# Performance work log

Measured on AMD Instinct MI355X. Metric: run time of the kernel, lower is better.

Reference implementation:

```python
import jax, jax.numpy as jnp
import numpy as np

N_NODES = 50000
N_EDGES = 800000
DIM = 128
BN_EPS = 1e-5  # torch.nn.BatchNorm1d default


def _lin_init(k, fan_in, fan_out):
    kw, kb = jax.random.split(k)
    s = 1.0 / np.sqrt(fan_in)
    W = jax.random.uniform(kw, (fan_in, fan_out), jnp.float32, -s, s)
    b = jax.random.uniform(kb, (fan_out,), jnp.float32, -s, s)
    return W, b


def setup_inputs() -> dict:
    key = jax.random.key(0)
    ks = jax.random.split(key, 8)
    d = {}
    d['h'] = jax.random.normal(ks[0], (N_NODES, DIM), jnp.float32)
    d['e'] = jax.random.normal(ks[1], (N_EDGES, DIM), jnp.float32)
    d['src'] = jax.random.randint(ks[2], (N_EDGES,), 0, N_NODES)
    d['dst'] = jax.random.randint(ks[3], (N_EDGES,), 0, N_NODES)
    # mlp_atom: Linear(128,128) -> ReLU -> Linear(128,128)
    d['Wa1'], d['ba1'] = _lin_init(ks[4], DIM, DIM)
    d['Wa2'], d['ba2'] = _lin_init(ks[5], DIM, DIM)
    # mlp_bond
    d['Wb1'], d['bb1'] = _lin_init(ks[6], DIM, DIM)
    d['Wb2'], d['bb2'] = _lin_init(ks[7], DIM, DIM)
    # BatchNorm1d affine params
    d['gamma_a'] = jnp.ones((DIM,), jnp.float32)
    d['beta_a'] = jnp.zeros((DIM,), jnp.float32)
    d['gamma_b'] = jnp.ones((DIM,), jnp.float32)
    d['beta_b'] = jnp.zeros((DIM,), jnp.float32)
    return d


def _mlp(x, W1, b1, W2, b2):
    return jax.nn.relu(x @ W1 + b1) @ W2 + b2


def _bn(x, gamma, beta):
    # training-mode batch norm over the node/edge axis
    mu = jnp.mean(x, axis=0)
    var = jnp.var(x, axis=0)
    return (x - mu) * jax.lax.rsqrt(var + BN_EPS) * gamma + beta


def reference(h, e, src, dst, Wa1, ba1, Wa2, ba2, Wb1, bb1, Wb2, bb2,
              gamma_a, beta_a, gamma_b, beta_b):
    # --- bond (edge) update: GIN-style sum of endpoint atom feats + bond feat
    me = h[src] + h[dst] + e                      # [E, D] irregular gather
    e_new = _bn(_mlp(me, Wb1, bb1, Wb2, bb2), gamma_b, beta_b)
    e_new = e_new + e                             # residual (dropout=Identity)
    # --- atom (node) update: sum-aggregate incident bond feats
    agg = jax.ops.segment_sum(e_new, dst, num_segments=N_NODES)  # [N, D] scatter
    h_new = _bn(_mlp(h + agg, Wa1, ba1, Wa2, ba2), gamma_a, beta_a)
    h_new = h_new + h                             # residual
    return h_new, e_new
```

## Files before the change

### kernel.cpp

```cpp
#include <hip/hip_runtime.h>
#include <cstddef>

#define NN 50000
#define NE 800000
#define D 128
#define BN_EPS 1e-5f

typedef __attribute__((ext_vector_type(8))) short bf16x8;
typedef __attribute__((ext_vector_type(4))) float f32x4;

union FragU { int4 i; bf16x8 v; };

__device__ __forceinline__ unsigned short f2bf(float x) {
    unsigned u = __float_as_uint(x);
    return (unsigned short)((u + 0x7fffu + ((u >> 16) & 1u)) >> 16);
}
__device__ __forceinline__ float bf2f(unsigned short b) {
    return __uint_as_float(((unsigned)b) << 16);
}
__device__ __forceinline__ unsigned pk2(float a, float b) {
    return (unsigned)f2bf(a) | ((unsigned)f2bf(b) << 16);
}

__global__ __launch_bounds__(256) void wprep_kernel(
    const float* __restrict__ W, unsigned short* __restrict__ Wt)
{
    const int idx = blockIdx.x * 256 + threadIdx.x;
    const int j  = idx & 7;
    const int l  = (idx >> 3) & 63;
    const int ks = (idx >> 9) & 3;
    const int ct = (idx >> 11) & 7;
    const int n  = 16 * ct + (l & 15);
    const int k  = 32 * ks + ((l >> 4) << 3) + j;
    Wt[idx] = f2bf(W[k * 128 + n]);
}

template<int MODE>
__global__ __launch_bounds__(256, 4) void mlp_mfma_kernel(
    const float* __restrict__ h, const float* __restrict__ e_or_agg,
    const int* __restrict__ src, const int* __restrict__ dst,
    const unsigned short* __restrict__ Wt1, const float* __restrict__ b1,
    const unsigned short* __restrict__ Wt2, const float* __restrict__ b2,
    float* __restrict__ x2out, float* __restrict__ stats)
{
    __shared__ __align__(16) unsigned short W1L[16384];
    __shared__ float red[1024];

    const int tid  = threadIdx.x;
    const int lane = tid & 63;
    const int w    = tid >> 6;
    const int g    = lane >> 4;
    const int m    = lane & 15;
    const long r0  = (long)blockIdx.x * 64;

    {
        int4* dp = (int4*)W1L;
        const int4* sp = (const int4*)Wt1;
#pragma unroll
        for (int i = 0; i < 8; ++i) dp[tid + 256 * i] = sp[tid + 256 * i];
    }
    __syncthreads();

    const long rowg = r0 + 16 * w + m;
    long rowl = rowg;
    if (MODE == 1) rowl = (rowl < NN) ? rowl : (NN - 1);

    const float *pa, *pb, *pc;
    if (MODE == 0) {
        pa = e_or_agg + (size_t)rowg * D;
        pb = h + (size_t)src[rowg] * D;
        pc = h + (size_t)dst[rowg] * D;
    } else {
        pa = h + (size_t)rowl * D;
        pb = e_or_agg + (size_t)rowl * D;
        pc = nullptr;
    }

    FragU xh[4], xl[4];
#pragma unroll
    for (int ks = 0; ks < 4; ++ks) {
        const int c = 32 * ks + 8 * g;
        const float4 aa = *(const float4*)(pa + c);
        const float4 ab = *(const float4*)(pa + c + 4);
        const float4 ba = *(const float4*)(pb + c);
        const float4 bb = *(const float4*)(pb + c + 4);
        float xs[8];
        xs[0] = aa.x + ba.x; xs[1] = aa.y + ba.y; xs[2] = aa.z + ba.z; xs[3] = aa.w + ba.w;
        xs[4] = ab.x + bb.x; xs[5] = ab.y + bb.y; xs[6] = ab.z + bb.z; xs[7] = ab.w + bb.w;
        if (MODE == 0) {
            const float4 ca = *(const float4*)(pc + c);
            const float4 cb = *(const float4*)(pc + c + 4);
            xs[0] += ca.x; xs[1] += ca.y; xs[2] += ca.z; xs[3] += ca.w;
            xs[4] += cb.x; xs[5] += cb.y; xs[6] += cb.z; xs[7] += cb.w;
        }
        const unsigned h0 = pk2(xs[0], xs[1]), h1 = pk2(xs[2], xs[3]);
        const unsigned h2 = pk2(xs[4], xs[5]), h3 = pk2(xs[6], xs[7]);
        xh[ks].i = make_int4(h0, h1, h2, h3);
        float lo[8];
        lo[0] = xs[0] - bf2f((unsigned short)h0);  lo[1] = xs[1] - bf2f((unsigned short)(h0 >> 16));
        lo[2] = xs[2] - bf2f((unsigned short)h1);  lo[3] = xs[3] - bf2f((unsigned short)(h1 >> 16));
        lo[4] = xs[4] - bf2f((unsigned short)h2);  lo[5] = xs[5] - bf2f((unsigned short)(h2 >> 16));
        lo[6] = xs[6] - bf2f((unsigned short)h3);  lo[7] = xs[7] - bf2f((unsigned short)(h3 >> 16));
        xl[ks].i = make_int4(pk2(lo[0], lo[1]), pk2(lo[2], lo[3]),
                             pk2(lo[4], lo[5]), pk2(lo[6], lo[7]));
    }

    const bf16x8* W1f = (const bf16x8*)W1L;
    f32x4 acc[8];
#pragma unroll
    for (int ct = 0; ct < 8; ++ct) acc[ct] = (f32x4){0.f, 0.f, 0.f, 0.f};
#pragma unroll
    for (int ct = 0; ct < 8; ++ct)
#pragma unroll
        for (int ks = 0; ks < 4; ++ks) {
            const bf16x8 wf = W1f[(ct * 4 + ks) * 64 + lane];
            acc[ct] = __builtin_amdgcn_mfma_f32_16x16x32_bf16(wf, xh[ks].v, acc[ct], 0, 0, 0);
            acc[ct] = __builtin_amdgcn_mfma_f32_16x16x32_bf16(wf, xl[ks].v, acc[ct], 0, 0, 0);
        }

    unsigned yh[8][2], yl[8][2];
#pragma unroll
    for (int ct = 0; ct < 8; ++ct) {
        const float4 bv = *(const float4*)(b1 + 16 * ct + 4 * g);
        const float y0 = fmaxf(acc[ct][0] + bv.x, 0.f);
        const float y1 = fmaxf(acc[ct][1] + bv.y, 0.f);
        const float y2 = fmaxf(acc[ct][2] + bv.z, 0.f);
        const float y3 = fmaxf(acc[ct][3] + bv.w, 0.f);
        yh[ct][0] = pk2(y0, y1);  yh[ct][1] = pk2(y2, y3);
        const float l0 = y0 - bf2f((unsigned short)yh[ct][0]);
        const float l1 = y1 - bf2f((unsigned short)(yh[ct][0] >> 16));
        const float l2 = y2 - bf2f((unsigned short)yh[ct][1]);
        const float l3 = y3 - bf2f((unsigned short)(yh[ct][1] >> 16));
        yl[ct][0] = pk2(l0, l1);  yl[ct][1] = pk2(l2, l3);
    }

    FragU ah[4], al[4];
    const int sA = ((g & 1) << 5) | m;
    const int sB = sA + 16;
    const bool gh = (g >> 1) != 0;
#pragma unroll
    for (int ks = 0; ks < 4; ++ks) {
        int p, q, w0, w1, w2, w3;
        p = __shfl((int)yh[2*ks][0], sA); q = __shfl((int)yh[2*ks+1][0], sA); w0 = gh ? q : p;
        p = __shfl((int)yh[2*ks][1], sA); q = __shfl((int)yh[2*ks+1][1], sA); w1 = gh ? q : p;
        p = __shfl((int)yh[2*ks][0], sB); q = __shfl((int)yh[2*ks+1][0], sB); w2 = gh ? q : p;
        p = __shfl((int)yh[2*ks][1], sB); q = __shfl((int)yh[2*ks+1][1], sB); w3 = gh ? q : p;
        ah[ks].i = make_int4(w0, w1, w2, w3);
        p = __shfl((int)yl[2*ks][0], sA); q = __shfl((int)yl[2*ks+1][0], sA); w0 = gh ? q : p;
        p = __shfl((int)yl[2*ks][1], sA); q = __shfl((int)yl[2*ks+1][1], sA); w1 = gh ? q : p;
        p = __shfl((int)yl[2*ks][0], sB); q = __shfl((int)yl[2*ks+1][0], sB); w2 = gh ? q : p;
        p = __shfl((int)yl[2*ks][1], sB); q = __shfl((int)yl[2*ks+1][1], sB); w3 = gh ? q : p;
        al[ks].i = make_int4(w0, w1, w2, w3);
    }

    const bf16x8* W2f = (const bf16x8*)Wt2;
    f32x4 acc2[8];
#pragma unroll
    for (int ct = 0; ct < 8; ++ct) acc2[ct] = (f32x4){0.f, 0.f, 0.f, 0.f};
#pragma unroll
    for (int ct = 0; ct < 8; ++ct)
#pragma unroll
        for (int ks = 0; ks < 4; ++ks) {
            const bf16x8 wf = W2f[(ct * 4 + ks) * 64 + lane];
            acc2[ct] = __builtin_amdgcn_mfma_f32_16x16x32_bf16(ah[ks].v, wf, acc2[ct], 0, 0, 0);
            acc2[ct] = __builtin_amdgcn_mfma_f32_16x16x32_bf16(al[ks].v, wf, acc2[ct], 0, 0, 0);
        }

#pragma unroll
    for (int ct = 0; ct < 8; ++ct) {
        const float b2c = b2[16 * ct + m];
        float s = 0.f, q = 0.f;
#pragma unroll
        for (int r = 0; r < 4; ++r) {
            const long grow = r0 + 16 * w + 4 * g + r;
            if (MODE == 0 || grow < NN) {
                const float z = acc2[ct][r] + b2c;
                x2out[(size_t)grow * D + 16 * ct + m] = z;
                s += z; q += z * z;
            }
        }
        s += __shfl_xor(s, 16); s += __shfl_xor(s, 32);
        q += __shfl_xor(q, 16); q += __shfl_xor(q, 32);
        if (g == 0) {
            red[w * 128 + 16 * ct + m]       = s;
            red[512 + w * 128 + 16 * ct + m] = q;
        }
    }
    __syncthreads();
    if (tid < 128) {
        const float s = red[tid] + red[128 + tid] + red[256 + tid] + red[384 + tid];
        const float q = red[512 + tid] + red[640 + tid] + red[768 + tid] + red[896 + tid];
        unsafeAtomicAdd(&stats[tid], s);
        unsafeAtomicAdd(&stats[128 + tid], q);
    }
}

__global__ void bn_finalize_kernel(float* __restrict__ stats,
                                   const float* __restrict__ gamma,
                                   const float* __restrict__ beta,
                                   float inv_count)
{
    const int c = threadIdx.x;
    if (c < D) {
        const float mu  = stats[c] * inv_count;
        const float var = stats[128 + c] * inv_count - mu * mu;
        const float sc  = rsqrtf(var + BN_EPS) * gamma[c];
        stats[256 + c] = sc;
        stats[384 + c] = beta[c] - mu * sc;
    }
}

__global__ __launch_bounds__(256) void hist_kernel(
    const int* __restrict__ dst, int* __restrict__ cnt)
{
    const int i = blockIdx.x * 256 + threadIdx.x;
    if (i < NE) atomicAdd(&cnt[dst[i]], 1);
}

__global__ __launch_bounds__(1024) void scan_kernel(
    const int* __restrict__ cnt, int* __restrict__ off)
{
    __shared__ int part[1024];
    const int t = threadIdx.x;
    const int SEG = (NN + 1023) / 1024;
    const int base = t * SEG;

    int s = 0;
    for (int i = 0; i < SEG; ++i) {
        const int idx = base + i;
        if (idx < NN) s += cnt[idx];
    }
    part[t] = s;
    __syncthreads();
    for (int d = 1; d < 1024; d <<= 1) {
        int v = (t >= d) ? part[t - d] : 0;
        __syncthreads();
        part[t] += v;
        __syncthreads();
    }
    int run = (t > 0) ? part[t - 1] : 0;
    for (int i = 0; i < SEG; ++i) {
        const int idx = base + i;
        if (idx < NN) { off[idx] = run; run += cnt[idx]; }
    }
    if (t == 1023) off[NN] = part[1023];
}

__global__ __launch_bounds__(256) void csr_scatter_kernel(
    const int* __restrict__ dst, const int* __restrict__ off,
    int* __restrict__ cnt, int* __restrict__ csr)
{
    const int i = blockIdx.x * 256 + threadIdx.x;
    if (i < NE) {
        const int d = dst[i];
        const int p = atomicSub(&cnt[d], 1) - 1;
        csr[off[d] + p] = i;
    }
}

__global__ __launch_bounds__(256) void apply_gather_kernel(
    const float* __restrict__ e, const float* __restrict__ stats,
    const int* __restrict__ off, const int* __restrict__ csr,
    float* __restrict__ eout, float* __restrict__ agg)
{
    const int node = blockIdx.x * 4 + (threadIdx.x >> 6);
    const int lane = threadIdx.x & 63;
    const int c0   = lane * 2;
    if (node >= NN) return;

    const float2 sc = *(const float2*)(stats + 256 + c0);
    const float2 sh = *(const float2*)(stats + 384 + c0);
    float2 acc = make_float2(0.f, 0.f);
    const int jb = off[node], je = off[node + 1];
    for (int j = jb; j < je; ++j) {
        const int eidx = csr[j];
        const size_t base = (size_t)eidx * D + c0;
        const float2 x  = *(const float2*)(eout + base);
        const float2 ev = *(const float2*)(e + base);
        float2 v;
        v.x = fmaf(x.x, sc.x, sh.x) + ev.x;
        v.y = fmaf(x.y, sc.y, sh.y) + ev.y;
        *(float2*)(eout + base) = v;
        acc.x += v.x;
        acc.y += v.y;
    }
    *(float2*)(agg + (size_t)node * D + c0) = acc;
}

__global__ __launch_bounds__(256) void node_apply_kernel(
    const float* __restrict__ h, const float* __restrict__ stats,
    float* __restrict__ hout)
{
    const int gid = blockIdx.x * 256 + threadIdx.x;
    const int c0  = (gid & 31) * 4;
    const size_t base = (size_t)(gid >> 5) * D + c0;

    const float4 sc = *(const float4*)(stats + 256 + c0);
    const float4 sh = *(const float4*)(stats + 384 + c0);
    const float4 x  = *(const float4*)(hout + base);
    const float4 hv = *(const float4*)(h + base);
    float4 v;
    v.x = fmaf(x.x, sc.x, sh.x) + hv.x;
    v.y = fmaf(x.y, sc.y, sh.y) + hv.y;
    v.z = fmaf(x.z, sc.z, sh.z) + hv.z;
    v.w = fmaf(x.w, sc.w, sh.w) + hv.w;
    *(float4*)(hout + base) = v;
}

extern "C" void kernel_launch(void* const* d_in, const int* in_sizes, int n_in,
                              void* d_out, int out_size, void* d_ws, size_t ws_size,
                              hipStream_t stream)
{
    const float* h   = (const float*)d_in[0];
    const float* e   = (const float*)d_in[1];
    const int*   src = (const int*)d_in[2];
    const int*   dst = (const int*)d_in[3];
    const float* Wa1 = (const float*)d_in[4];
    const float* ba1 = (const float*)d_in[5];
    const float* Wa2 = (const float*)d_in[6];
    const float* ba2 = (const float*)d_in[7];
    const float* Wb1 = (const float*)d_in[8];
    const float* bb1 = (const float*)d_in[9];
    const float* Wb2 = (const float*)d_in[10];
    const float* bb2 = (const float*)d_in[11];
    const float* ga  = (const float*)d_in[12];
    const float* bea = (const float*)d_in[13];
    const float* gb  = (const float*)d_in[14];
    const float* beb = (const float*)d_in[15];

    float* out  = (float*)d_out;
    float* hnew = out;
    float* enew = out + (size_t)NN * D;

    float* ws     = (float*)d_ws;
    float* estats = ws;
    float* nstats = ws + 512;
    int*   icnt   = (int*)(ws + 1024);
    int*   ioff   = icnt + NN;
    unsigned short* wtb1 = (unsigned short*)(ioff + NN + 1 + 3);
    unsigned short* wtb2 = wtb1 + 16384;
    unsigned short* wta1 = wtb2 + 16384;
    unsigned short* wta2 = wta1 + 16384;
    int*   icsr  = (int*)(wta2 + 16384);
    float* agg   = (float*)(icsr + NE);

    hipMemsetAsync(d_ws, 0, (size_t)(1024 + NN) * sizeof(float), stream);

    wprep_kernel<<<64, 256, 0, stream>>>(Wb1, wtb1);
    wprep_kernel<<<64, 256, 0, stream>>>(Wb2, wtb2);
    wprep_kernel<<<64, 256, 0, stream>>>(Wa1, wta1);
    wprep_kernel<<<64, 256, 0, stream>>>(Wa2, wta2);

    hist_kernel<<<(NE + 255) / 256, 256, 0, stream>>>(dst, icnt);
    scan_kernel<<<1, 1024, 0, stream>>>(icnt, ioff);
    csr_scatter_kernel<<<(NE + 255) / 256, 256, 0, stream>>>(dst, ioff, icnt, icsr);

    mlp_mfma_kernel<0><<<NE / 64, 256, 0, stream>>>(h, e, src, dst,
                                                    wtb1, bb1, wtb2, bb2,
                                                    enew , estats);
    bn_finalize_kernel<<<1, 128, 0, stream>>>(estats, gb, beb, 1.0f / NE);
    apply_gather_kernel<<<(NN + 3) / 4, 256, 0, stream>>>(e, estats, ioff, icsr,
                                                          enew, agg);

    mlp_mfma_kernel<1><<<(NN + 63) / 64, 256, 0, stream>>>(h, agg, nullptr, nullptr,
                                                           wta1, ba1, wta2, ba2,
                                                           hnew , nstats);
    bn_finalize_kernel<<<1, 128, 0, stream>>>(nstats, ga, bea, 1.0f / NN);
    node_apply_kernel<<<(NN * 32) / 256, 256, 0, stream>>>(h, nstats, hnew);
}
```

Measured before the change: 868.4 us.

## Process four row tiles per wave with double-buffered gather loads and LDS-resident W2

Each block now handles 256 rows: every wave runs four 16-row tiles. The raw gather loads for the next tile are issued before computing the current one (two register buffers), which hides the latency of the irregular loads. W2 is also staged in LDS alongside W1, and the BN partial sums are accumulated across tiles, so there are fewer blocks, fewer atomics and less repeated weight staging. The cost is heavy register use: launch bounds drop to 2 blocks per CU and 48 float4 raw buffers are held, so occupancy falls and spilling is possible. The node kernel also gets coarser work with a tail of clamped rows.

```diff
diff --git a/kernel.cpp b/kernel.cpp
--- a/kernel.cpp
+++ b/kernel.cpp
@@ -35,8 +35,135 @@
     Wt[idx] = f2bf(W[k * 128 + n]);
 }
 
+#define LOAD_TILE(TT, RAW)                                                     \
+    {                                                                          \
+        long rowg = r0w + (TT) * 16 + m;                                       \
+        if (MODE == 1 && rowg >= NN) rowg = NN - 1;                            \
+        const float *pa, *pb, *pc = nullptr;                                   \
+        if (MODE == 0) {                                                       \
+            pa = e_or_agg + (size_t)rowg * D;                                  \
+            pb = h + (size_t)src[rowg] * D;                                    \
+            pc = h + (size_t)dst[rowg] * D;                                    \
+        } else {                                                               \
+            pa = h + (size_t)rowg * D;                                         \
+            pb = e_or_agg + (size_t)rowg * D;                                  \
+        }                                                                      \
+        _Pragma("unroll")                                                      \
+        for (int ks = 0; ks < 4; ++ks) {                                       \
+            const int c = 32 * ks + 8 * g;                                     \
+            RAW[ks * 6 + 0] = *(const float4*)(pa + c);                        \
+            RAW[ks * 6 + 1] = *(const float4*)(pa + c + 4);                    \
+            RAW[ks * 6 + 2] = *(const float4*)(pb + c);                        \
+            RAW[ks * 6 + 3] = *(const float4*)(pb + c + 4);                    \
+            if (MODE == 0) {                                                   \
+                RAW[ks * 6 + 4] = *(const float4*)(pc + c);                    \
+                RAW[ks * 6 + 5] = *(const float4*)(pc + c + 4);                \
+            }                                                                  \
+        }                                                                      \
+    }
+
+#define COMPUTE_TILE(TT, RAW)                                                  \
+    {                                                                          \
+        FragU xh[4], xl[4];                                                    \
+        _Pragma("unroll")                                                      \
+        for (int ks = 0; ks < 4; ++ks) {                                       \
+            const float4 aa = RAW[ks * 6 + 0], ab = RAW[ks * 6 + 1];           \
+            const float4 ba = RAW[ks * 6 + 2], bb = RAW[ks * 6 + 3];           \
+            float xs[8];                                                       \
+            xs[0] = aa.x + ba.x; xs[1] = aa.y + ba.y;                          \
+            xs[2] = aa.z + ba.z; xs[3] = aa.w + ba.w;                          \
+            xs[4] = ab.x + bb.x; xs[5] = ab.y + bb.y;                          \
+            xs[6] = ab.z + bb.z; xs[7] = ab.w + bb.w;                          \
+            if (MODE == 0) {                                                   \
+                const float4 ca = RAW[ks * 6 + 4], cb = RAW[ks * 6 + 5];       \
+                xs[0] += ca.x; xs[1] += ca.y; xs[2] += ca.z; xs[3] += ca.w;    \
+                xs[4] += cb.x; xs[5] += cb.y; xs[6] += cb.z; xs[7] += cb.w;    \
+            }                                                                  \
+            const unsigned h0 = pk2(xs[0], xs[1]), h1 = pk2(xs[2], xs[3]);     \
+            const unsigned h2 = pk2(xs[4], xs[5]), h3 = pk2(xs[6], xs[7]);     \
+            xh[ks].i = make_int4(h0, h1, h2, h3);                              \
+            xl[ks].i = make_int4(                                              \
+                pk2(xs[0] - bf2f((unsigned short)h0),                          \
+                    xs[1] - bf2f((unsigned short)(h0 >> 16))),                 \
+                pk2(xs[2] - bf2f((unsigned short)h1),                          \
+                    xs[3] - bf2f((unsigned short)(h1 >> 16))),                 \
+                pk2(xs[4] - bf2f((unsigned short)h2),                          \
+                    xs[5] - bf2f((unsigned short)(h2 >> 16))),                 \
+                pk2(xs[6] - bf2f((unsigned short)h3),                          \
+                    xs[7] - bf2f((unsigned short)(h3 >> 16))));                \
+        }                                                                      \
+        f32x4 acc[8];                                                          \
+        _Pragma("unroll")                                                      \
+        for (int ct = 0; ct < 8; ++ct) acc[ct] = (f32x4){0.f, 0.f, 0.f, 0.f}; \
+        _Pragma("unroll")                                                      \
+        for (int ct = 0; ct < 8; ++ct)                                         \
+            _Pragma("unroll")                                                  \
+            for (int ks = 0; ks < 4; ++ks) {                                   \
+                const bf16x8 wf = W1f[(ct * 4 + ks) * 64 + lane];              \
+                acc[ct] = __builtin_amdgcn_mfma_f32_16x16x32_bf16(             \
+                    wf, xh[ks].v, acc[ct], 0, 0, 0);                           \
+                acc[ct] = __builtin_amdgcn_mfma_f32_16x16x32_bf16(             \
+                    wf, xl[ks].v, acc[ct], 0, 0, 0);                           \
+            }                                                                  \
+        unsigned yh[8][2], yl[8][2];                                           \
+        _Pragma("unroll")                                                      \
+        for (int ct = 0; ct < 8; ++ct) {                                       \
+            const float4 bv = *(const float4*)(b1 + 16 * ct + 4 * g);          \
+            const float y0 = fmaxf(acc[ct][0] + bv.x, 0.f);                    \
+            const float y1 = fmaxf(acc[ct][1] + bv.y, 0.f);                    \
+            const float y2 = fmaxf(acc[ct][2] + bv.z, 0.f);                    \
+            const float y3 = fmaxf(acc[ct][3] + bv.w, 0.f);                    \
+            yh[ct][0] = pk2(y0, y1);  yh[ct][1] = pk2(y2, y3);                 \
+            yl[ct][0] = pk2(y0 - bf2f((unsigned short)yh[ct][0]),              \
+                            y1 - bf2f((unsigned short)(yh[ct][0] >> 16)));     \
+            yl[ct][1] = pk2(y2 - bf2f((unsigned short)yh[ct][1]),              \
+                            y3 - bf2f((unsigned short)(yh[ct][1] >> 16)));     \
+        }                                                                      \
+        FragU ah[4], al[4];                                                    \
+        _Pragma("unroll")                                                      \
+        for (int ks = 0; ks < 4; ++ks) {                                       \
+            int p, q, w0, w1, w2, w3;                                          \
+            p = __shfl((int)yh[2*ks][0], sA); q = __shfl((int)yh[2*ks+1][0], sA); w0 = gh ? q : p; \
+            p = __shfl((int)yh[2*ks][1], sA); q = __shfl((int)yh[2*ks+1][1], sA); w1 = gh ? q : p; \
+            p = __shfl((int)yh[2*ks][0], sB); q = __shfl((int)yh[2*ks+1][0], sB); w2 = gh ? q : p; \
+            p = __shfl((int)yh[2*ks][1], sB); q = __shfl((int)yh[2*ks+1][1], sB); w3 = gh ? q : p; \
+            ah[ks].i = make_int4(w0, w1, w2, w3);                              \
+            p = __shfl((int)yl[2*ks][0], sA); q = __shfl((int)yl[2*ks+1][0], sA); w0 = gh ? q : p; \
+            p = __shfl((int)yl[2*ks][1], sA); q = __shfl((int)yl[2*ks+1][1], sA); w1 = gh ? q : p; \
+            p = __shfl((int)yl[2*ks][0], sB); q = __shfl((int)yl[2*ks+1][0], sB); w2 = gh ? q : p; \
+            p = __shfl((int)yl[2*ks][1], sB); q = __shfl((int)yl[2*ks+1][1], sB); w3 = gh ? q : p; \
+            al[ks].i = make_int4(w0, w1, w2, w3);                              \
+        }                                                                      \
+        f32x4 acc2[8];                                                         \
+        _Pragma("unroll")                                                      \
+        for (int ct = 0; ct < 8; ++ct) acc2[ct] = (f32x4){0.f, 0.f, 0.f, 0.f};\
+        _Pragma("unroll")                                                      \
+        for (int ct = 0; ct < 8; ++ct)                                         \
+            _Pragma("unroll")                                                  \
+            for (int ks = 0; ks < 4; ++ks) {                                   \
+                const bf16x8 wf = W2f[(ct * 4 + ks) * 64 + lane];              \
+                acc2[ct] = __builtin_amdgcn_mfma_f32_16x16x32_bf16(            \
+                    ah[ks].v, wf, acc2[ct], 0, 0, 0);                          \
+                acc2[ct] = __builtin_amdgcn_mfma_f32_16x16x32_bf16(            \
+                    al[ks].v, wf, acc2[ct], 0, 0, 0);                          \
+            }                                                                  \
+        _Pragma("unroll")                                                      \
+        for (int ct = 0; ct < 8; ++ct) {                                       \
+            const float b2c = b2[16 * ct + m];                                 \
+            _Pragma("unroll")                                                  \
+            for (int r = 0; r < 4; ++r) {                                      \
+                const long grow = r0w + (TT) * 16 + 4 * g + r;                 \
+                if (MODE == 0 || grow < NN) {                                  \
+                    const float z = acc2[ct][r] + b2c;                         \
+                    x2out[(size_t)grow * D + 16 * ct + m] = z;                 \
+                    sAcc[ct] += z; qAcc[ct] += z * z;                          \
+                }                                                              \
+            }                                                                  \
+        }                                                                      \
+    }
+
 template<int MODE>
-__global__ __launch_bounds__(256, 4) void mlp_mfma_kernel(
+__global__ __launch_bounds__(256, 2) void mlp_mfma_kernel(
     const float* __restrict__ h, const float* __restrict__ e_or_agg,
     const int* __restrict__ src, const int* __restrict__ dst,
     const unsigned short* __restrict__ Wt1, const float* __restrict__ b1,
@@ -44,6 +171,7 @@
     float* __restrict__ x2out, float* __restrict__ stats)
 {
     __shared__ __align__(16) unsigned short W1L[16384];
+    __shared__ __align__(16) unsigned short W2L[16384];
     __shared__ float red[1024];
 
     const int tid  = threadIdx.x;
@@ -51,134 +179,42 @@
     const int w    = tid >> 6;
     const int g    = lane >> 4;
     const int m    = lane & 15;
-    const long r0  = (long)blockIdx.x * 64;
+    const long r0w = (long)blockIdx.x * 256 + 64 * w;
 
     {
-        int4* dp = (int4*)W1L;
-        const int4* sp = (const int4*)Wt1;
+        int4* d1 = (int4*)W1L;  const int4* s1 = (const int4*)Wt1;
+        int4* d2 = (int4*)W2L;  const int4* s2 = (const int4*)Wt2;
 #pragma unroll
-        for (int i = 0; i < 8; ++i) dp[tid + 256 * i] = sp[tid + 256 * i];
+        for (int i = 0; i < 8; ++i) {
+            d1[tid + 256 * i] = s1[tid + 256 * i];
+            d2[tid + 256 * i] = s2[tid + 256 * i];
+        }
     }
     __syncthreads();
 
-    const long rowg = r0 + 16 * w + m;
-    long rowl = rowg;
-    if (MODE == 1) rowl = (rowl < NN) ? rowl : (NN - 1);
-
-    const float *pa, *pb, *pc;
-    if (MODE == 0) {
-        pa = e_or_agg + (size_t)rowg * D;
-        pb = h + (size_t)src[rowg] * D;
-        pc = h + (size_t)dst[rowg] * D;
-    } else {
-        pa = h + (size_t)rowl * D;
-        pb = e_or_agg + (size_t)rowl * D;
-        pc = nullptr;
-    }
-
-    FragU xh[4], xl[4];
-#pragma unroll
-    for (int ks = 0; ks < 4; ++ks) {
-        const int c = 32 * ks + 8 * g;
-        const float4 aa = *(const float4*)(pa + c);
-        const float4 ab = *(const float4*)(pa + c + 4);
-        const float4 ba = *(const float4*)(pb + c);
-        const float4 bb = *(const float4*)(pb + c + 4);
-        float xs[8];
-        xs[0] = aa.x + ba.x; xs[1] = aa.y + ba.y; xs[2] = aa.z + ba.z; xs[3] = aa.w + ba.w;
-        xs[4] = ab.x + bb.x; xs[5] = ab.y + bb.y; xs[6] = ab.z + bb.z; xs[7] = ab.w + bb.w;
-        if (MODE == 0) {
-            const float4 ca = *(const float4*)(pc + c);
-            const float4 cb = *(const float4*)(pc + c + 4);
-            xs[0] += ca.x; xs[1] += ca.y; xs[2] += ca.z; xs[3] += ca.w;
-            xs[4] += cb.x; xs[5] += cb.y; xs[6] += cb.z; xs[7] += cb.w;
-        }
-        const unsigned h0 = pk2(xs[0], xs[1]), h1 = pk2(xs[2], xs[3]);
-        const unsigned h2 = pk2(xs[4], xs[5]), h3 = pk2(xs[6], xs[7]);
-        xh[ks].i = make_int4(h0, h1, h2, h3);
-        float lo[8];
-        lo[0] = xs[0] - bf2f((unsigned short)h0);  lo[1] = xs[1] - bf2f((unsigned short)(h0 >> 16));
-        lo[2] = xs[2] - bf2f((unsigned short)h1);  lo[3] = xs[3] - bf2f((unsigned short)(h1 >> 16));
-        lo[4] = xs[4] - bf2f((unsigned short)h2);  lo[5] = xs[5] - bf2f((unsigned short)(h2 >> 16));
-        lo[6] = xs[6] - bf2f((unsigned short)h3);  lo[7] = xs[7] - bf2f((unsigned short)(h3 >> 16));
-        xl[ks].i = make_int4(pk2(lo[0], lo[1]), pk2(lo[2], lo[3]),
-                             pk2(lo[4], lo[5]), pk2(lo[6], lo[7]));
-    }
-
     const bf16x8* W1f = (const bf16x8*)W1L;
-    f32x4 acc[8];
-#pragma unroll
-    for (int ct = 0; ct < 8; ++ct) acc[ct] = (f32x4){0.f, 0.f, 0.f, 0.f};
-#pragma unroll
-    for (int ct = 0; ct < 8; ++ct)
-#pragma unroll
-        for (int ks = 0; ks < 4; ++ks) {
-            const bf16x8 wf = W1f[(ct * 4 + ks) * 64 + lane];
-            acc[ct] = __builtin_amdgcn_mfma_f32_16x16x32_bf16(wf, xh[ks].v, acc[ct], 0, 0, 0);
-            acc[ct] = __builtin_amdgcn_mfma_f32_16x16x32_bf16(wf, xl[ks].v, acc[ct], 0, 0, 0);
-        }
-
-    unsigned yh[8][2], yl[8][2];
-#pragma unroll
-    for (int ct = 0; ct < 8; ++ct) {
-        const float4 bv = *(const float4*)(b1 + 16 * ct + 4 * g);
-        const float y0 = fmaxf(acc[ct][0] + bv.x, 0.f);
-        const float y1 = fmaxf(acc[ct][1] + bv.y, 0.f);
-        const float y2 = fmaxf(acc[ct][2] + bv.z, 0.f);
-        const float y3 = fmaxf(acc[ct][3] + bv.w, 0.f);
-        yh[ct][0] = pk2(y0, y1);  yh[ct][1] = pk2(y2, y3);
-        const float l0 = y0 - bf2f((unsigned short)yh[ct][0]);
-        const float l1 = y1 - bf2f((unsigned short)(yh[ct][0] >> 16));
-        const float l2 = y2 - bf2f((unsigned short)yh[ct][1]);
-        const float l3 = y3 - bf2f((unsigned short)(yh[ct][1] >> 16));
-        yl[ct][0] = pk2(l0, l1);  yl[ct][1] = pk2(l2, l3);
-    }
-
-    FragU ah[4], al[4];
+    const bf16x8* W2f = (const bf16x8*)W2L;
     const int sA = ((g & 1) << 5) | m;
     const int sB = sA + 16;
     const bool gh = (g >> 1) != 0;
+
+    float sAcc[8], qAcc[8];
 #pragma unroll
-    for (int ks = 0; ks < 4; ++ks) {
-        int p, q, w0, w1, w2, w3;
-        p = __shfl((int)yh[2*ks][0], sA); q = __shfl((int)yh[2*ks+1][0], sA); w0 = gh ? q : p;
-        p = __shfl((int)yh[2*ks][1], sA); q = __shfl((int)yh[2*ks+1][1], sA); w1 = gh ? q : p;
-        p = __shfl((int)yh[2*ks][0], sB); q = __shfl((int)yh[2*ks+1][0], sB); w2 = gh ? q : p;
-        p = __shfl((int)yh[2*ks][1], sB); q = __shfl((int)yh[2*ks+1][1], sB); w3 = gh ? q : p;
-        ah[ks].i = make_int4(w0, w1, w2, w3);
-        p = __shfl((int)yl[2*ks][0], sA); q = __shfl((int)yl[2*ks+1][0], sA); w0 = gh ? q : p;
-        p = __shfl((int)yl[2*ks][1], sA); q = __shfl((int)yl[2*ks+1][1], sA); w1 = gh ? q : p;
-        p = __shfl((int)yl[2*ks][0], sB); q = __shfl((int)yl[2*ks+1][0], sB); w2 = gh ? q : p;
-        p = __shfl((int)yl[2*ks][1], sB); q = __shfl((int)yl[2*ks+1][1], sB); w3 = gh ? q : p;
-        al[ks].i = make_int4(w0, w1, w2, w3);
-    }
-
-    const bf16x8* W2f = (const bf16x8*)Wt2;
-    f32x4 acc2[8];
-#pragma unroll
-    for (int ct = 0; ct < 8; ++ct) acc2[ct] = (f32x4){0.f, 0.f, 0.f, 0.f};
-#pragma unroll
-    for (int ct = 0; ct < 8; ++ct)
-#pragma unroll
-        for (int ks = 0; ks < 4; ++ks) {
-            const bf16x8 wf = W2f[(ct * 4 + ks) * 64 + lane];
-            acc2[ct] = __builtin_amdgcn_mfma_f32_16x16x32_bf16(ah[ks].v, wf, acc2[ct], 0, 0, 0);
-            acc2[ct] = __builtin_amdgcn_mfma_f32_16x16x32_bf16(al[ks].v, wf, acc2[ct], 0, 0, 0);
-        }
+    for (int ct = 0; ct < 8; ++ct) { sAcc[ct] = 0.f; qAcc[ct] = 0.f; }
+
+    float4 rawA[24], rawB[24];
+    LOAD_TILE(0, rawA)
+    LOAD_TILE(1, rawB)
+    COMPUTE_TILE(0, rawA)
+    LOAD_TILE(2, rawA)
+    COMPUTE_TILE(1, rawB)
+    LOAD_TILE(3, rawB)
+    COMPUTE_TILE(2, rawA)
+    COMPUTE_TILE(3, rawB)
 
 #pragma unroll
     for (int ct = 0; ct < 8; ++ct) {
-        const float b2c = b2[16 * ct + m];
-        float s = 0.f, q = 0.f;
-#pragma unroll
-        for (int r = 0; r < 4; ++r) {
-            const long grow = r0 + 16 * w + 4 * g + r;
-            if (MODE == 0 || grow < NN) {
-                const float z = acc2[ct][r] + b2c;
-                x2out[(size_t)grow * D + 16 * ct + m] = z;
-                s += z; q += z * z;
-            }
-        }
+        float s = sAcc[ct], q = qAcc[ct];
         s += __shfl_xor(s, 16); s += __shfl_xor(s, 32);
         q += __shfl_xor(q, 16); q += __shfl_xor(q, 32);
         if (g == 0) {
@@ -355,16 +391,16 @@
     scan_kernel<<<1, 1024, 0, stream>>>(icnt, ioff);
     csr_scatter_kernel<<<(NE + 255) / 256, 256, 0, stream>>>(dst, ioff, icnt, icsr);
 
-    mlp_mfma_kernel<0><<<NE / 64, 256, 0, stream>>>(h, e, src, dst,
-                                                    wtb1, bb1, wtb2, bb2,
-                                                    enew , estats);
+    mlp_mfma_kernel<0><<<NE / 256, 256, 0, stream>>>(h, e, src, dst,
+                                                     wtb1, bb1, wtb2, bb2,
+                                                     enew , estats);
     bn_finalize_kernel<<<1, 128, 0, stream>>>(estats, gb, beb, 1.0f / NE);
     apply_gather_kernel<<<(NN + 3) / 4, 256, 0, stream>>>(e, estats, ioff, icsr,
                                                           enew, agg);
 
-    mlp_mfma_kernel<1><<<(NN + 63) / 64, 256, 0, stream>>>(h, agg, nullptr, nullptr,
-                                                           wta1, ba1, wta2, ba2,
-                                                           hnew , nstats);
+    mlp_mfma_kernel<1><<<(NN + 255) / 256, 256, 0, stream>>>(h, agg, nullptr, nullptr,
+                                                             wta1, ba1, wta2, ba2,
+                                                             hnew , nstats);
     bn_finalize_kernel<<<1, 128, 0, stream>>>(nstats, ga, bea, 1.0f / NN);
     node_apply_kernel<<<(NN * 32) / 256, 256, 0, stream>>>(h, nstats, hnew);
 }
```

Result: slower. 904.4 us (+4.1%).

## Permute W1 columns to drop shuffles, stage W2 in LDS, split BN stats pass

Applied to the files above, without the earlier changes.

Layer-1 weight columns and bias are permuted so each lane's MFMA output already sits in the layout layer 2 needs as its B operand, which removes the cross-lane shuffles between the two GEMMs. W2 is now staged in LDS alongside W1. Blocks grow to 512 threads and each wave loops over four 16-row tiles. Column statistics move out of the MLP kernel into a separate col_stats pass that re-reads the output, and the apply-gather loop is unrolled by two. The stats pass adds a full extra read of the edge output in exchange for a simpler MLP epilogue with float4 stores.

```diff
diff --git a/kernel.cpp b/kernel.cpp
--- a/kernel.cpp
+++ b/kernel.cpp
@@ -20,6 +20,10 @@
 }
 __device__ __forceinline__ unsigned pk2(float a, float b) {
     return (unsigned)f2bf(a) | ((unsigned)f2bf(b) << 16);
+}
+
+__device__ __forceinline__ int pi_perm(int ct, int s) {
+    return 32 * (ct & 3) + 8 * (s >> 2) + 4 * (ct >> 2) + (s & 3);
 }
 
 __global__ __launch_bounds__(256) void wprep_kernel(
@@ -35,163 +39,197 @@
     Wt[idx] = f2bf(W[k * 128 + n]);
 }
 
+__global__ __launch_bounds__(256) void wprep_pi_kernel(
+    const float* __restrict__ W, unsigned short* __restrict__ Wt)
+{
+    const int idx = blockIdx.x * 256 + threadIdx.x;
+    const int j  = idx & 7;
+    const int l  = (idx >> 3) & 63;
+    const int ks = (idx >> 9) & 3;
+    const int ct = (idx >> 11) & 7;
+    const int n  = pi_perm(ct, l & 15);
+    const int k  = 32 * ks + ((l >> 4) << 3) + j;
+    Wt[idx] = f2bf(W[k * 128 + n]);
+}
+
+__global__ void bprep_kernel(const float* __restrict__ b, float* __restrict__ bp)
+{
+    const int p = threadIdx.x;
+    bp[p] = b[pi_perm(p >> 4, p & 15)];
+}
+
 template<int MODE>
-__global__ __launch_bounds__(256, 4) void mlp_mfma_kernel(
+__global__ __launch_bounds__(512, 2) void mlp_mfma_kernel(
     const float* __restrict__ h, const float* __restrict__ e_or_agg,
     const int* __restrict__ src, const int* __restrict__ dst,
-    const unsigned short* __restrict__ Wt1, const float* __restrict__ b1,
+    const unsigned short* __restrict__ Wt1, const float* __restrict__ b1p,
     const unsigned short* __restrict__ Wt2, const float* __restrict__ b2,
-    float* __restrict__ x2out, float* __restrict__ stats)
+    float* __restrict__ x2out)
 {
     __shared__ __align__(16) unsigned short W1L[16384];
-    __shared__ float red[1024];
+    __shared__ __align__(16) unsigned short W2L[16384];
 
     const int tid  = threadIdx.x;
     const int lane = tid & 63;
     const int w    = tid >> 6;
     const int g    = lane >> 4;
     const int m    = lane & 15;
-    const long r0  = (long)blockIdx.x * 64;
+    const long ROWS = (MODE == 0) ? NE : NN;
+    const long blockBase = (long)blockIdx.x * 512;
 
     {
-        int4* dp = (int4*)W1L;
-        const int4* sp = (const int4*)Wt1;
-#pragma unroll
-        for (int i = 0; i < 8; ++i) dp[tid + 256 * i] = sp[tid + 256 * i];
+        int4* d1 = (int4*)W1L;  const int4* s1 = (const int4*)Wt1;
+        int4* d2 = (int4*)W2L;  const int4* s2 = (const int4*)Wt2;
+#pragma unroll
+        for (int i = 0; i < 4; ++i) {
+            d1[tid + 512 * i] = s1[tid + 512 * i];
+            d2[tid + 512 * i] = s2[tid + 512 * i];
+        }
     }
     __syncthreads();
-
-    const long rowg = r0 + 16 * w + m;
-    long rowl = rowg;
-    if (MODE == 1) rowl = (rowl < NN) ? rowl : (NN - 1);
-
-    const float *pa, *pb, *pc;
-    if (MODE == 0) {
-        pa = e_or_agg + (size_t)rowg * D;
-        pb = h + (size_t)src[rowg] * D;
-        pc = h + (size_t)dst[rowg] * D;
-    } else {
-        pa = h + (size_t)rowl * D;
-        pb = e_or_agg + (size_t)rowl * D;
-        pc = nullptr;
-    }
-
-    FragU xh[4], xl[4];
-#pragma unroll
-    for (int ks = 0; ks < 4; ++ks) {
-        const int c = 32 * ks + 8 * g;
-        const float4 aa = *(const float4*)(pa + c);
-        const float4 ab = *(const float4*)(pa + c + 4);
-        const float4 ba = *(const float4*)(pb + c);
-        const float4 bb = *(const float4*)(pb + c + 4);
-        float xs[8];
-        xs[0] = aa.x + ba.x; xs[1] = aa.y + ba.y; xs[2] = aa.z + ba.z; xs[3] = aa.w + ba.w;
-        xs[4] = ab.x + bb.x; xs[5] = ab.y + bb.y; xs[6] = ab.z + bb.z; xs[7] = ab.w + bb.w;
+    const bf16x8* W1f = (const bf16x8*)W1L;
+    const bf16x8* W2f = (const bf16x8*)W2L;
+
+#pragma unroll 1
+    for (int t = 0; t < 4; ++t) {
+        const long rowg = blockBase + 64 * w + 16 * t + m;
+        const long rowc = (rowg < ROWS) ? rowg : (ROWS - 1);
+
+        const float *pa, *pb, *pc = nullptr;
         if (MODE == 0) {
-            const float4 ca = *(const float4*)(pc + c);
-            const float4 cb = *(const float4*)(pc + c + 4);
-            xs[0] += ca.x; xs[1] += ca.y; xs[2] += ca.z; xs[3] += ca.w;
-            xs[4] += cb.x; xs[5] += cb.y; xs[6] += cb.z; xs[7] += cb.w;
-        }
-        const unsigned h0 = pk2(xs[0], xs[1]), h1 = pk2(xs[2], xs[3]);
-        const unsigned h2 = pk2(xs[4], xs[5]), h3 = pk2(xs[6], xs[7]);
-        xh[ks].i = make_int4(h0, h1, h2, h3);
-        float lo[8];
-        lo[0] = xs[0] - bf2f((unsigned short)h0);  lo[1] = xs[1] - bf2f((unsigned short)(h0 >> 16));
-        lo[2] = xs[2] - bf2f((unsigned short)h1);  lo[3] = xs[3] - bf2f((unsigned short)(h1 >> 16));
-        lo[4] = xs[4] - bf2f((unsigned short)h2);  lo[5] = xs[5] - bf2f((unsigned short)(h2 >> 16));
-        lo[6] = xs[6] - bf2f((unsigned short)h3);  lo[7] = xs[7] - bf2f((unsigned short)(h3 >> 16));
-        xl[ks].i = make_int4(pk2(lo[0], lo[1]), pk2(lo[2], lo[3]),
-                             pk2(lo[4], lo[5]), pk2(lo[6], lo[7]));
-    }
-
-    const bf16x8* W1f = (const bf16x8*)W1L;
-    f32x4 acc[8];
-#pragma unroll
-    for (int ct = 0; ct < 8; ++ct) acc[ct] = (f32x4){0.f, 0.f, 0.f, 0.f};
-#pragma unroll
-    for (int ct = 0; ct < 8; ++ct)
+            pa = e_or_agg + (size_t)rowc * D;
+            pb = h + (size_t)src[rowc] * D;
+            pc = h + (size_t)dst[rowc] * D;
+        } else {
+            pa = h + (size_t)rowc * D;
+            pb = e_or_agg + (size_t)rowc * D;
+        }
+
+        FragU xh[4], xl[4];
 #pragma unroll
         for (int ks = 0; ks < 4; ++ks) {
-            const bf16x8 wf = W1f[(ct * 4 + ks) * 64 + lane];
-            acc[ct] = __builtin_amdgcn_mfma_f32_16x16x32_bf16(wf, xh[ks].v, acc[ct], 0, 0, 0);
-            acc[ct] = __builtin_amdgcn_mfma_f32_16x16x32_bf16(wf, xl[ks].v, acc[ct], 0, 0, 0);
-        }
-
-    unsigned yh[8][2], yl[8][2];
-#pragma unroll
-    for (int ct = 0; ct < 8; ++ct) {
-        const float4 bv = *(const float4*)(b1 + 16 * ct + 4 * g);
-        const float y0 = fmaxf(acc[ct][0] + bv.x, 0.f);
-        const float y1 = fmaxf(acc[ct][1] + bv.y, 0.f);
-        const float y2 = fmaxf(acc[ct][2] + bv.z, 0.f);
-        const float y3 = fmaxf(acc[ct][3] + bv.w, 0.f);
-        yh[ct][0] = pk2(y0, y1);  yh[ct][1] = pk2(y2, y3);
-        const float l0 = y0 - bf2f((unsigned short)yh[ct][0]);
-        const float l1 = y1 - bf2f((unsigned short)(yh[ct][0] >> 16));
-        const float l2 = y2 - bf2f((unsigned short)yh[ct][1]);
-        const float l3 = y3 - bf2f((unsigned short)(yh[ct][1] >> 16));
-        yl[ct][0] = pk2(l0, l1);  yl[ct][1] = pk2(l2, l3);
-    }
-
-    FragU ah[4], al[4];
-    const int sA = ((g & 1) << 5) | m;
-    const int sB = sA + 16;
-    const bool gh = (g >> 1) != 0;
-#pragma unroll
-    for (int ks = 0; ks < 4; ++ks) {
-        int p, q, w0, w1, w2, w3;
-        p = __shfl((int)yh[2*ks][0], sA); q = __shfl((int)yh[2*ks+1][0], sA); w0 = gh ? q : p;
-        p = __shfl((int)yh[2*ks][1], sA); q = __shfl((int)yh[2*ks+1][1], sA); w1 = gh ? q : p;
-        p = __shfl((int)yh[2*ks][0], sB); q = __shfl((int)yh[2*ks+1][0], sB); w2 = gh ? q : p;
-        p = __shfl((int)yh[2*ks][1], sB); q = __shfl((int)yh[2*ks+1][1], sB); w3 = gh ? q : p;
-        ah[ks].i = make_int4(w0, w1, w2, w3);
-        p = __shfl((int)yl[2*ks][0], sA); q = __shfl((int)yl[2*ks+1][0], sA); w0 = gh ? q : p;
-        p = __shfl((int)yl[2*ks][1], sA); q = __shfl((int)yl[2*ks+1][1], sA); w1 = gh ? q : p;
-        p = __shfl((int)yl[2*ks][0], sB); q = __shfl((int)yl[2*ks+1][0], sB); w2 = gh ? q : p;
-        p = __shfl((int)yl[2*ks][1], sB); q = __shfl((int)yl[2*ks+1][1], sB); w3 = gh ? q : p;
-        al[ks].i = make_int4(w0, w1, w2, w3);
-    }
-
-    const bf16x8* W2f = (const bf16x8*)Wt2;
-    f32x4 acc2[8];
-#pragma unroll
-    for (int ct = 0; ct < 8; ++ct) acc2[ct] = (f32x4){0.f, 0.f, 0.f, 0.f};
-#pragma unroll
-    for (int ct = 0; ct < 8; ++ct)
-#pragma unroll
-        for (int ks = 0; ks < 4; ++ks) {
-            const bf16x8 wf = W2f[(ct * 4 + ks) * 64 + lane];
-            acc2[ct] = __builtin_amdgcn_mfma_f32_16x16x32_bf16(ah[ks].v, wf, acc2[ct], 0, 0, 0);
-            acc2[ct] = __builtin_amdgcn_mfma_f32_16x16x32_bf16(al[ks].v, wf, acc2[ct], 0, 0, 0);
-        }
-
-#pragma unroll
-    for (int ct = 0; ct < 8; ++ct) {
-        const float b2c = b2[16 * ct + m];
-        float s = 0.f, q = 0.f;
-#pragma unroll
-        for (int r = 0; r < 4; ++r) {
-            const long grow = r0 + 16 * w + 4 * g + r;
-            if (MODE == 0 || grow < NN) {
-                const float z = acc2[ct][r] + b2c;
-                x2out[(size_t)grow * D + 16 * ct + m] = z;
-                s += z; q += z * z;
+            const int c = 32 * ks + 8 * g;
+            const float4 aa = *(const float4*)(pa + c);
+            const float4 ab = *(const float4*)(pa + c + 4);
+            const float4 ba = *(const float4*)(pb + c);
+            const float4 bb = *(const float4*)(pb + c + 4);
+            float xs[8];
+            xs[0] = aa.x + ba.x; xs[1] = aa.y + ba.y;
+            xs[2] = aa.z + ba.z; xs[3] = aa.w + ba.w;
+            xs[4] = ab.x + bb.x; xs[5] = ab.y + bb.y;
+            xs[6] = ab.z + bb.z; xs[7] = ab.w + bb.w;
+            if (MODE == 0) {
+                const float4 ca = *(const float4*)(pc + c);
+                const float4 cb = *(const float4*)(pc + c + 4);
+                xs[0] += ca.x; xs[1] += ca.y; xs[2] += ca.z; xs[3] += ca.w;
+                xs[4] += cb.x; xs[5] += cb.y; xs[6] += cb.z; xs[7] += cb.w;
             }
-        }
-        s += __shfl_xor(s, 16); s += __shfl_xor(s, 32);
-        q += __shfl_xor(q, 16); q += __shfl_xor(q, 32);
-        if (g == 0) {
-            red[w * 128 + 16 * ct + m]       = s;
-            red[512 + w * 128 + 16 * ct + m] = q;
-        }
-    }
+            const unsigned h0 = pk2(xs[0], xs[1]), h1 = pk2(xs[2], xs[3]);
+            const unsigned h2 = pk2(xs[4], xs[5]), h3 = pk2(xs[6], xs[7]);
+            xh[ks].i = make_int4(h0, h1, h2, h3);
+            xl[ks].i = make_int4(
+                pk2(xs[0] - bf2f((unsigned short)h0),
+                    xs[1] - bf2f((unsigned short)(h0 >> 16))),
+                pk2(xs[2] - bf2f((unsigned short)h1),
+                    xs[3] - bf2f((unsigned short)(h1 >> 16))),
+                pk2(xs[4] - bf2f((unsigned short)h2),
+                    xs[5] - bf2f((unsigned short)(h2 >> 16))),
+                pk2(xs[6] - bf2f((unsigned short)h3),
+                    xs[7] - bf2f((unsigned short)(h3 >> 16))));
+        }
+
+        f32x4 acc[8];
+#pragma unroll
+        for (int ct = 0; ct < 8; ++ct) acc[ct] = (f32x4){0.f, 0.f, 0.f, 0.f};
+#pragma unroll
+        for (int ct = 0; ct < 8; ++ct)
+#pragma unroll
+            for (int ks = 0; ks < 4; ++ks) {
+                const bf16x8 wf = W1f[(ct * 4 + ks) * 64 + lane];
+                acc[ct] = __builtin_amdgcn_mfma_f32_16x16x32_bf16(wf, xh[ks].v, acc[ct], 0, 0, 0);
+                acc[ct] = __builtin_amdgcn_mfma_f32_16x16x32_bf16(wf, xl[ks].v, acc[ct], 0, 0, 0);
+            }
+
+        FragU yh[4], yl[4];
+#pragma unroll
+        for (int ks2 = 0; ks2 < 4; ++ks2) {
+            const float4 bva = *(const float4*)(b1p + 16 * ks2 + 4 * g);
+            const float4 bvb = *(const float4*)(b1p + 16 * (ks2 + 4) + 4 * g);
+            const float y0 = fmaxf(acc[ks2][0] + bva.x, 0.f);
+            const float y1 = fmaxf(acc[ks2][1] + bva.y, 0.f);
+            const float y2 = fmaxf(acc[ks2][2] + bva.z, 0.f);
+            const float y3 = fmaxf(acc[ks2][3] + bva.w, 0.f);
+            const float y4 = fmaxf(acc[ks2 + 4][0] + bvb.x, 0.f);
+            const float y5 = fmaxf(acc[ks2 + 4][1] + bvb.y, 0.f);
+            const float y6 = fmaxf(acc[ks2 + 4][2] + bvb.z, 0.f);
+            const float y7 = fmaxf(acc[ks2 + 4][3] + bvb.w, 0.f);
+            const unsigned u0 = pk2(y0, y1), u1 = pk2(y2, y3);
+            const unsigned u2 = pk2(y4, y5), u3 = pk2(y6, y7);
+            yh[ks2].i = make_int4(u0, u1, u2, u3);
+            yl[ks2].i = make_int4(
+                pk2(y0 - bf2f((unsigned short)u0), y1 - bf2f((unsigned short)(u0 >> 16))),
+                pk2(y2 - bf2f((unsigned short)u1), y3 - bf2f((unsigned short)(u1 >> 16))),
+                pk2(y4 - bf2f((unsigned short)u2), y5 - bf2f((unsigned short)(u2 >> 16))),
+                pk2(y6 - bf2f((unsigned short)u3), y7 - bf2f((unsigned short)(u3 >> 16))));
+        }
+
+        f32x4 acc2[8];
+#pragma unroll
+        for (int ct2 = 0; ct2 < 8; ++ct2) acc2[ct2] = (f32x4){0.f, 0.f, 0.f, 0.f};
+#pragma unroll
+        for (int ct2 = 0; ct2 < 8; ++ct2)
+#pragma unroll
+            for (int ks2 = 0; ks2 < 4; ++ks2) {
+                const bf16x8 wf = W2f[(ct2 * 4 + ks2) * 64 + lane];
+                acc2[ct2] = __builtin_amdgcn_mfma_f32_16x16x32_bf16(wf, yh[ks2].v, acc2[ct2], 0, 0, 0);
+                acc2[ct2] = __builtin_amdgcn_mfma_f32_16x16x32_bf16(wf, yl[ks2].v, acc2[ct2], 0, 0, 0);
+            }
+
+        if (rowg < ROWS) {
+            float* orow = x2out + (size_t)rowg * D;
+#pragma unroll
+            for (int ct2 = 0; ct2 < 8; ++ct2) {
+                const float4 bv = *(const float4*)(b2 + 16 * ct2 + 4 * g);
+                float4 v;
+                v.x = acc2[ct2][0] + bv.x;
+                v.y = acc2[ct2][1] + bv.y;
+                v.z = acc2[ct2][2] + bv.z;
+                v.w = acc2[ct2][3] + bv.w;
+                *(float4*)(orow + 16 * ct2 + 4 * g) = v;
+            }
+        }
+    }
+}
+
+__global__ __launch_bounds__(256) void col_stats_kernel(
+    const float* __restrict__ x, long rows, float* __restrict__ stats)
+{
+    __shared__ float red[2048];
+    const int tid = threadIdx.x;
+    const int cg  = tid & 31;
+    const int rg  = tid >> 5;
+    const int c0  = cg * 4;
+
+    float4 s = make_float4(0.f, 0.f, 0.f, 0.f);
+    float4 q = make_float4(0.f, 0.f, 0.f, 0.f);
+    for (long r = (long)blockIdx.x * 8 + rg; r < rows; r += (long)gridDim.x * 8) {
+        const float4 v = *(const float4*)(x + r * D + c0);
+        s.x += v.x; s.y += v.y; s.z += v.z; s.w += v.w;
+        q.x += v.x * v.x; q.y += v.y * v.y;
+        q.z += v.z * v.z; q.w += v.w * v.w;
+    }
+    *(float4*)&red[rg * 128 + c0]        = s;
+    *(float4*)&red[1024 + rg * 128 + c0] = q;
     __syncthreads();
     if (tid < 128) {
-        const float s = red[tid] + red[128 + tid] + red[256 + tid] + red[384 + tid];
-        const float q = red[512 + tid] + red[640 + tid] + red[768 + tid] + red[896 + tid];
-        unsafeAtomicAdd(&stats[tid], s);
-        unsafeAtomicAdd(&stats[128 + tid], q);
+        float ss = 0.f, qq = 0.f;
+#pragma unroll
+        for (int i = 0; i < 8; ++i) {
+            ss += red[i * 128 + tid];
+            qq += red[1024 + i * 128 + tid];
+        }
+        unsafeAtomicAdd(&stats[tid], ss);
+        unsafeAtomicAdd(&stats[128 + tid], qq);
     }
 }
 
@@ -272,17 +310,37 @@
     const float2 sh = *(const float2*)(stats + 384 + c0);
     float2 acc = make_float2(0.f, 0.f);
     const int jb = off[node], je = off[node + 1];
-    for (int j = jb; j < je; ++j) {
-        const int eidx = csr[j];
-        const size_t base = (size_t)eidx * D + c0;
-        const float2 x  = *(const float2*)(eout + base);
-        const float2 ev = *(const float2*)(e + base);
-        float2 v;
-        v.x = fmaf(x.x, sc.x, sh.x) + ev.x;
-        v.y = fmaf(x.y, sc.y, sh.y) + ev.y;
-        *(float2*)(eout + base) = v;
-        acc.x += v.x;
-        acc.y += v.y;
+    int j = jb;
+    for (; j + 2 <= je; j += 2) {
+        const int e0 = csr[j];
+        const int e1 = csr[j + 1];
+        const size_t b0 = (size_t)e0 * D + c0;
+        const size_t b1 = (size_t)e1 * D + c0;
+        const float2 x0  = *(const float2*)(eout + b0);
+        const float2 ev0 = *(const float2*)(e + b0);
+        const float2 x1  = *(const float2*)(eout + b1);
+        const float2 ev1 = *(const float2*)(e + b1);
+        float2 v0, v1;
+        v0.x = fmaf(x0.x, sc.x, sh.x) + ev0.x;
+        v0.y = fmaf(x0.y, sc.y, sh.y) + ev0.y;
+        v1.x = fmaf(x1.x, sc.x, sh.x) + ev1.x;
+        v1.y = fmaf(x1.y, sc.y, sh.y) + ev1.y;
+        *(float2*)(eout + b0) = v0;
+        *(float2*)(eout + b1) = v1;
+        acc.x += v0.x + v1.x;
+        acc.y += v0.y + v1.y;
+    }
+    if (j < je) {
+        const int e0 = csr[j];
+        const size_t b0 = (size_t)e0 * D + c0;
+        const float2 x0  = *(const float2*)(eout + b0);
+        const float2 ev0 = *(const float2*)(e + b0);
+        float2 v0;
+        v0.x = fmaf(x0.x, sc.x, sh.x) + ev0.x;
+        v0.y = fmaf(x0.y, sc.y, sh.y) + ev0.y;
+        *(float2*)(eout + b0) = v0;
+        acc.x += v0.x;
+        acc.y += v0.y;
     }
     *(float2*)(agg + (size_t)node * D + c0) = acc;
 }
@@ -337,7 +395,9 @@
     float* nstats = ws + 512;
     int*   icnt   = (int*)(ws + 1024);
     int*   ioff   = icnt + NN;
-    unsigned short* wtb1 = (unsigned short*)(ioff + NN + 1 + 3);
+    float* b1pe   = (float*)(ioff + NN + 1 + 3);
+    float* b1pn   = b1pe + 128;
+    unsigned short* wtb1 = (unsigned short*)(b1pn + 128);
     unsigned short* wtb2 = wtb1 + 16384;
     unsigned short* wta1 = wtb2 + 16384;
     unsigned short* wta2 = wta1 + 16384;
@@ -346,25 +406,27 @@
 
     hipMemsetAsync(d_ws, 0, (size_t)(1024 + NN) * sizeof(float), stream);
 
-    wprep_kernel<<<64, 256, 0, stream>>>(Wb1, wtb1);
+    wprep_pi_kernel<<<64, 256, 0, stream>>>(Wb1, wtb1);
     wprep_kernel<<<64, 256, 0, stream>>>(Wb2, wtb2);
-    wprep_kernel<<<64, 256, 0, stream>>>(Wa1, wta1);
+    wprep_pi_kernel<<<64, 256, 0, stream>>>(Wa1, wta1);
     wprep_kernel<<<64, 256, 0, stream>>>(Wa2, wta2);
+    bprep_kernel<<<1, 128, 0, stream>>>(bb1, b1pe);
+    bprep_kernel<<<1, 128, 0, stream>>>(ba1, b1pn);
 
     hist_kernel<<<(NE + 255) / 256, 256, 0, stream>>>(dst, icnt);
     scan_kernel<<<1, 1024, 0, stream>>>(icnt, ioff);
     csr_scatter_kernel<<<(NE + 255) / 256, 256, 0, stream>>>(dst, ioff, icnt, icsr);
 
-    mlp_mfma_kernel<0><<<NE / 64, 256, 0, stream>>>(h, e, src, dst,
-                                                    wtb1, bb1, wtb2, bb2,
-                                                    enew , estats);
+    mlp_mfma_kernel<0><<<(NE + 511) / 512, 512, 0, stream>>>(
+        h, e, src, dst, wtb1, b1pe, wtb2, bb2, enew );
+    col_stats_kernel<<<2048, 256, 0, stream>>>(enew, (long)NE, estats);
     bn_finalize_kernel<<<1, 128, 0, stream>>>(estats, gb, beb, 1.0f / NE);
     apply_gather_kernel<<<(NN + 3) / 4, 256, 0, stream>>>(e, estats, ioff, icsr,
                                                           enew, agg);
 
-    mlp_mfma_kernel<1><<<(NN + 63) / 64, 256, 0, stream>>>(h, agg, nullptr, nullptr,
-                                                           wta1, ba1, wta2, ba2,
-                                                           hnew , nstats);
+    mlp_mfma_kernel<1><<<(NN + 511) / 512, 512, 0, stream>>>(
+        h, agg, nullptr, nullptr, wta1, b1pn, wta2, ba2, hnew );
+    col_stats_kernel<<<256, 256, 0, stream>>>(hnew, (long)NN, nstats);
     bn_finalize_kernel<<<1, 128, 0, stream>>>(nstats, ga, bea, 1.0f / NN);
     node_apply_kernel<<<(NN * 32) / 256, 256, 0, stream>>>(h, nstats, hnew);
 }
```

Measured after the change: 1.338 ms. 54.1% more time.
